# Performance work log

Hardware: AMD Instinct MI355X
Metric: run time of the kernel (lower is better)

The kernel has to match this reference:

```python
import jax, jax.numpy as jnp
import numpy as np

B, I, H = 65536, 512, 128
T, ES, EC = 2, 2, 4  # tasks, specific experts per task, common experts
ETOT = ES + EC


def setup_inputs() -> dict:
    key = jax.random.key(0)
    ks = jax.random.split(key, 9)
    s = 0.02
    return {
        "x": jax.random.normal(ks[0], (B, I), dtype=jnp.float32),
        "Wc": jax.random.normal(ks[1], (EC, I, H), dtype=jnp.float32) * s,
        "bc": jax.random.normal(ks[2], (EC, H), dtype=jnp.float32) * s,
        "Ws": jax.random.normal(ks[3], (T, ES, I, H), dtype=jnp.float32) * s,
        "bs": jax.random.normal(ks[4], (T, ES, H), dtype=jnp.float32) * s,
        "Wg": jax.random.normal(ks[5], (T, ETOT * H, ETOT), dtype=jnp.float32) * s,
        "bg": jax.random.normal(ks[6], (T, ETOT), dtype=jnp.float32) * s,
        "Wt": jax.random.normal(ks[7], (T, H, 1), dtype=jnp.float32) * s,
        "bt": jax.random.normal(ks[8], (T, 1), dtype=jnp.float32) * s,
    }


def reference(x, Wc, bc, Ws, bs, Wg, bg, Wt, bt):
    # Common experts: [EC, B, H]
    common = jnp.einsum("bi,eih->ebh", x, Wc) + bc[:, None, :]
    # Task-specific experts: [T, ES, B, H]
    spec = jnp.einsum("bi,teih->tebh", x, Ws) + bs[:, :, None, :]
    # Per task: experts ordered [specific..., common...] -> [T, ETOT, B, H]
    tmp = jnp.concatenate(
        [spec, jnp.broadcast_to(common[None], (T,) + common.shape)], axis=1
    )
    # Gate input: per-sample concat of all expert outputs -> [T, B, ETOT*H]
    gate_in = tmp.transpose(0, 2, 1, 3).reshape(T, B, ETOT * H)
    weights = jax.nn.softmax(
        jnp.einsum("tbf,tfe->tbe", gate_in, Wg) + bg[:, None, :], axis=-1
    )  # [T, B, ETOT]
    feature = jnp.einsum("tbe,tebh->tbh", weights, tmp)  # [T, B, H]
    out = jnp.einsum("tbh,tho->tbo", feature, Wt) + bt[:, None, :]  # [T, B, 1]
    return out
```

## Files before the change

### kernel.cpp

```cpp
#include <hip/hip_runtime.h>
#include <math.h>

#define BB 65536
#define II 512
#define HH 128
#define TT 2
#define ES 2
#define EC 4
#define NS 6
#define NJ 12
#define NCOL 24
#define FF (NS * HH)

#define PF 8

__global__ __launch_bounds__(256) void cgc_precompute(
    const float* __restrict__ Wc, const float* __restrict__ bc,
    const float* __restrict__ Ws, const float* __restrict__ bs,
    const float* __restrict__ Wg, const float* __restrict__ bg,
    const float* __restrict__ Wt,
    float* __restrict__ M, float* __restrict__ d)
{
    __shared__ float wrow[TT * FF];
    __shared__ float wg[TT * FF * NS];
    __shared__ float wt[TT * HH];
    __shared__ float red[NCOL][PF + 1];

    const int blk = blockIdx.x;
    const bool isd = (blk == II);
    const int i   = blk;
    const int tid = threadIdx.x;

    {
        const float4* Wg4 = (const float4*)Wg;
        float4* wg4 = (float4*)wg;
        for (int idx = tid; idx < TT * FF * NS / 4; idx += 256)
            wg4[idx] = Wg4[idx];
        if (tid < TT * HH / 4)
            ((float4*)wt)[tid] = ((const float4*)Wt)[tid];
    }
    {
        const float4* Ws4 = (const float4*)Ws;
        const float4* Wc4 = (const float4*)Wc;
        const float4* bs4 = (const float4*)bs;
        const float4* bc4 = (const float4*)bc;
        float4* wr4 = (float4*)wrow;
        for (int idx = tid; idx < TT * FF / 4; idx += 256) {
            const int t   = idx / (FF / 4);
            const int rem = idx % (FF / 4);
            const int s   = rem >> 5;
            const int h4  = rem & 31;
            float4 v;
            if (isd) {
                v = (s < ES) ? bs4[(t * ES + s) * 32 + h4]
                             : bc4[(s - ES) * 32 + h4];
            } else {
                v = (s < ES) ? Ws4[((t * ES + s) * II + i) * 32 + h4]
                             : Wc4[((s - ES) * II + i) * 32 + h4];
            }
            wr4[idx] = v;
        }
    }
    __syncthreads();

    const int col = tid >> 3;
    const int fp  = tid & 7;
    if (col < NCOL) {
        const int t = col / NJ;
        const int j = col % NJ;
        float acc = 0.0f;
        if (j < NS) {
            const float* wr  = &wrow[t * FF];
            const float* wgr = &wg[t * FF * NS + j];
            const int f0 = fp * 96;
            #pragma unroll 4
            for (int f = f0; f < f0 + 96; ++f)
                acc = fmaf(wr[f], wgr[f * NS], acc);
        } else {
            const int s = j - NS;
            const float* wr  = &wrow[t * FF + s * HH];
            const float* wtr = &wt[t * HH];
            const int h0 = fp * 16;
            #pragma unroll
            for (int h = h0; h < h0 + 16; ++h)
                acc = fmaf(wr[h], wtr[h], acc);
        }
        red[col][fp] = acc;
    }
    __syncthreads();

    if (tid < NCOL) {
        float v = 0.0f;
        #pragma unroll
        for (int p = 0; p < PF; ++p) v += red[tid][p];
        const int t = tid / NJ, j = tid % NJ;
        if (isd) {
            if (j < NS) v += bg[t * NS + j];
            d[tid] = v;
        } else {
            M[i * NCOL + tid] = v;
        }
    }
}

#define ROWS 64
#define WV 4
#define KW (II / WV)
#define KC 32
#define NCHUNK (KW / KC)
#define LPAD (ROWS + 1)
#define ZPAD 25
#define MCH (KC * NCOL)

union MainSh {
    float tile[WV][KC][LPAD];
    float zbuf[WV][ROWS][ZPAD];
};

__global__ __launch_bounds__(256) void cgc_main(
    const float* __restrict__ x,
    const float* __restrict__ Mg,
    const float* __restrict__ dg,
    const float* __restrict__ bt,
    float* __restrict__ out)
{
    __shared__ MainSh sh;
    __shared__ float mt[WV][MCH];

    const int tid  = threadIdx.x;
    const int w    = tid >> 6;
    const int lane = tid & 63;
    const int r0   = blockIdx.x * ROWS;
    const int row  = r0 + lane;
    const int lr   = lane >> 3;
    const int lk   = (lane & 7) * 4;
    const int kw0  = w * KW;

    const float4* xv = (const float4*)x;
    const float4* mg4 = (const float4*)Mg;
    float4 pre[8];
    float4 mpre[3];

    auto load_chunk = [&](int c) {
        const int kbase = kw0 + c * KC + lk;
        #pragma unroll
        for (int it = 0; it < 8; ++it) {
            const int rr = r0 + lr + it * 8;
            pre[it] = xv[(rr * II + kbase) >> 2];
        }
        const int mb4 = (kw0 + c * KC) * (NCOL / 4);
        #pragma unroll
        for (int r = 0; r < 3; ++r)
            mpre[r] = mg4[mb4 + r * 64 + lane];
    };
    auto store_chunk = [&]() {
        #pragma unroll
        for (int it = 0; it < 8; ++it) {
            const int rr = lr + it * 8;
            sh.tile[w][lk + 0][rr] = pre[it].x;
            sh.tile[w][lk + 1][rr] = pre[it].y;
            sh.tile[w][lk + 2][rr] = pre[it].z;
            sh.tile[w][lk + 3][rr] = pre[it].w;
        }
        float4* m4 = (float4*)&mt[w][0];
        #pragma unroll
        for (int r = 0; r < 3; ++r)
            m4[r * 64 + lane] = mpre[r];
    };

    float z[NCOL];
    #pragma unroll
    for (int j = 0; j < NCOL; ++j) z[j] = (w == 0) ? dg[j] : 0.0f;

    load_chunk(0);
    store_chunk();
    __builtin_amdgcn_wave_barrier();

    #pragma unroll 1
    for (int c = 0; c < NCHUNK; ++c) {
        if (c + 1 < NCHUNK) load_chunk(c + 1);

        #pragma unroll 2
        for (int k = 0; k < KC; ++k) {
            const float xk = sh.tile[w][k][lane];
            const float4* mr = (const float4*)&mt[w][k * NCOL];
            #pragma unroll
            for (int jq = 0; jq < 6; ++jq) {
                const float4 mv = mr[jq];
                z[jq * 4 + 0] = fmaf(xk, mv.x, z[jq * 4 + 0]);
                z[jq * 4 + 1] = fmaf(xk, mv.y, z[jq * 4 + 1]);
                z[jq * 4 + 2] = fmaf(xk, mv.z, z[jq * 4 + 2]);
                z[jq * 4 + 3] = fmaf(xk, mv.w, z[jq * 4 + 3]);
            }
        }

        __builtin_amdgcn_wave_barrier();
        if (c + 1 < NCHUNK) {
            store_chunk();
            __builtin_amdgcn_wave_barrier();
        }
    }

    __syncthreads();
    if (w > 0) {
        #pragma unroll
        for (int j = 0; j < NCOL; ++j) sh.zbuf[w][lane][j] = z[j];
    }
    __syncthreads();

    if (w == 0) {
        #pragma unroll
        for (int ww = 1; ww < WV; ++ww)
            #pragma unroll
            for (int j = 0; j < NCOL; ++j)
                z[j] += sh.zbuf[ww][lane][j];

        #pragma unroll
        for (int t = 0; t < TT; ++t) {
            const int base = t * NJ;
            float m = z[base + 0];
            #pragma unroll
            for (int j = 1; j < NS; ++j) m = fmaxf(m, z[base + j]);
            float s = 0.0f, o = 0.0f;
            #pragma unroll
            for (int j = 0; j < NS; ++j) {
                const float e = __expf(z[base + j] - m);
                s += e;
                o += e * z[base + NS + j];
            }
            out[t * BB + row] = o / s + bt[t];
        }
    }
}

extern "C" void kernel_launch(void* const* d_in, const int* in_sizes, int n_in,
                              void* d_out, int out_size, void* d_ws, size_t ws_size,
                              hipStream_t stream)
{
    const float* x  = (const float*)d_in[0];
    const float* Wc = (const float*)d_in[1];
    const float* bc = (const float*)d_in[2];
    const float* Ws = (const float*)d_in[3];
    const float* bs = (const float*)d_in[4];
    const float* Wg = (const float*)d_in[5];
    const float* bg = (const float*)d_in[6];
    const float* Wt = (const float*)d_in[7];
    const float* bt = (const float*)d_in[8];
    float* out = (float*)d_out;

    float* M = (float*)d_ws;
    float* d = M + II * NCOL;

    cgc_precompute<<<dim3(II + 1), dim3(256), 0, stream>>>(
        Wc, bc, Ws, bs, Wg, bg, Wt, M, d);
    cgc_main<<<dim3(BB / ROWS), dim3(256), 0, stream>>>(
        x, M, d, bt, out);
}
```

Baseline: 231.1 us.

## Read folded weight matrix via scalar loads and transpose gate weights in LDS

The main kernel stops staging the folded M matrix through shared memory. It marks the wave's k-offset as wave-uniform with readfirstlane so that M rows can be fetched with scalar (SMEM) loads straight from global memory, which removes per-chunk LDS stores and vector LDS reads from the inner FMA loop. The precompute kernel transposes the gate weights into a padded LDS layout and interleaves the partial-sum indices across threads to cut bank conflicts. The risk is that scalar load latency in the hot loop may not be hidden, and the unroll is raised to 4.

```diff
diff --git a/kernel.cpp b/kernel.cpp
--- a/kernel.cpp
+++ b/kernel.cpp
@@ -12,7 +12,7 @@
 #define NCOL 24
 #define FF (NS * HH)
 
-#define PF 8
+#define FFP (FF + 4)
 
 __global__ __launch_bounds__(256) void cgc_precompute(
     const float* __restrict__ Wc, const float* __restrict__ bc,
@@ -22,9 +22,9 @@
     float* __restrict__ M, float* __restrict__ d)
 {
     __shared__ float wrow[TT * FF];
-    __shared__ float wg[TT * FF * NS];
+    __shared__ float wgt[TT * NS * FFP];
     __shared__ float wt[TT * HH];
-    __shared__ float red[NCOL][PF + 1];
+    __shared__ float red[NCOL][9];
 
     const int blk = blockIdx.x;
     const bool isd = (blk == II);
@@ -33,9 +33,20 @@
 
     {
         const float4* Wg4 = (const float4*)Wg;
-        float4* wg4 = (float4*)wg;
-        for (int idx = tid; idx < TT * FF * NS / 4; idx += 256)
-            wg4[idx] = Wg4[idx];
+        for (int idx = tid; idx < TT * FF * NS / 4; idx += 256) {
+            const float4 v = Wg4[idx];
+            const int p0 = idx * 4;
+            const float vv[4] = {v.x, v.y, v.z, v.w};
+            #pragma unroll
+            for (int u = 0; u < 4; ++u) {
+                const int p = p0 + u;
+                const int t = p / (FF * NS);
+                const int r = p % (FF * NS);
+                const int f = r / NS;
+                const int e = r % NS;
+                wgt[(t * NS + e) * FFP + f] = vv[u];
+            }
+        }
         if (tid < TT * HH / 4)
             ((float4*)wt)[tid] = ((const float4*)Wt)[tid];
     }
@@ -71,19 +82,21 @@
         float acc = 0.0f;
         if (j < NS) {
             const float* wr  = &wrow[t * FF];
-            const float* wgr = &wg[t * FF * NS + j];
-            const int f0 = fp * 96;
+            const float* wgr = &wgt[(t * NS + j) * FFP];
             #pragma unroll 4
-            for (int f = f0; f < f0 + 96; ++f)
-                acc = fmaf(wr[f], wgr[f * NS], acc);
+            for (int ff = 0; ff < FF / 8; ++ff) {
+                const int f = ff * 8 + fp;
+                acc = fmaf(wr[f], wgr[f], acc);
+            }
         } else {
             const int s = j - NS;
             const float* wr  = &wrow[t * FF + s * HH];
             const float* wtr = &wt[t * HH];
-            const int h0 = fp * 16;
-            #pragma unroll
-            for (int h = h0; h < h0 + 16; ++h)
+            #pragma unroll
+            for (int hh = 0; hh < HH / 8; ++hh) {
+                const int h = hh * 8 + fp;
                 acc = fmaf(wr[h], wtr[h], acc);
+            }
         }
         red[col][fp] = acc;
     }
@@ -92,7 +105,7 @@
     if (tid < NCOL) {
         float v = 0.0f;
         #pragma unroll
-        for (int p = 0; p < PF; ++p) v += red[tid][p];
+        for (int p = 0; p < 8; ++p) v += red[tid][p];
         const int t = tid / NJ, j = tid % NJ;
         if (isd) {
             if (j < NS) v += bg[t * NS + j];
@@ -110,7 +123,6 @@
 #define NCHUNK (KW / KC)
 #define LPAD (ROWS + 1)
 #define ZPAD 25
-#define MCH (KC * NCOL)
 
 union MainSh {
     float tile[WV][KC][LPAD];
@@ -125,7 +137,6 @@
     float* __restrict__ out)
 {
     __shared__ MainSh sh;
-    __shared__ float mt[WV][MCH];
 
     const int tid  = threadIdx.x;
     const int w    = tid >> 6;
@@ -134,12 +145,10 @@
     const int row  = r0 + lane;
     const int lr   = lane >> 3;
     const int lk   = (lane & 7) * 4;
-    const int kw0  = w * KW;
+    const int kw0  = __builtin_amdgcn_readfirstlane(w * KW);
 
     const float4* xv = (const float4*)x;
-    const float4* mg4 = (const float4*)Mg;
     float4 pre[8];
-    float4 mpre[3];
 
     auto load_chunk = [&](int c) {
         const int kbase = kw0 + c * KC + lk;
@@ -148,10 +157,6 @@
             const int rr = r0 + lr + it * 8;
             pre[it] = xv[(rr * II + kbase) >> 2];
         }
-        const int mb4 = (kw0 + c * KC) * (NCOL / 4);
-        #pragma unroll
-        for (int r = 0; r < 3; ++r)
-            mpre[r] = mg4[mb4 + r * 64 + lane];
     };
     auto store_chunk = [&]() {
         #pragma unroll
@@ -162,10 +167,6 @@
             sh.tile[w][lk + 2][rr] = pre[it].z;
             sh.tile[w][lk + 3][rr] = pre[it].w;
         }
-        float4* m4 = (float4*)&mt[w][0];
-        #pragma unroll
-        for (int r = 0; r < 3; ++r)
-            m4[r * 64 + lane] = mpre[r];
     };
 
     float z[NCOL];
@@ -180,18 +181,14 @@
     for (int c = 0; c < NCHUNK; ++c) {
         if (c + 1 < NCHUNK) load_chunk(c + 1);
 
-        #pragma unroll 2
+        const float* Mc = Mg + (kw0 + c * KC) * NCOL;
+        #pragma unroll 4
         for (int k = 0; k < KC; ++k) {
             const float xk = sh.tile[w][k][lane];
-            const float4* mr = (const float4*)&mt[w][k * NCOL];
-            #pragma unroll
-            for (int jq = 0; jq < 6; ++jq) {
-                const float4 mv = mr[jq];
-                z[jq * 4 + 0] = fmaf(xk, mv.x, z[jq * 4 + 0]);
-                z[jq * 4 + 1] = fmaf(xk, mv.y, z[jq * 4 + 1]);
-                z[jq * 4 + 2] = fmaf(xk, mv.z, z[jq * 4 + 2]);
-                z[jq * 4 + 3] = fmaf(xk, mv.w, z[jq * 4 + 3]);
-            }
+            const float* Mr = Mc + k * NCOL;
+            #pragma unroll
+            for (int j = 0; j < NCOL; ++j)
+                z[j] = fmaf(xk, Mr[j], z[j]);
         }
 
         __builtin_amdgcn_wave_barrier();
```

Result: faster. 222.8 us (-3.6%).
